# Kernel optimization log

Hardware: AMD Instinct MI355X
Metric: run time of the kernel (lower is better)

The kernel has to match this reference:

```python
import jax, jax.numpy as jnp
import numpy as np

BN_EPS = 1e-5


def setup_inputs() -> dict:
    key = jax.random.key(0)
    ks = jax.random.split(key, 10)
    d = {}
    # EEG-style input: [B, 1, T, electrodes]
    d["x"] = jax.random.normal(ks[0], (512, 1, 1125, 5), dtype=jnp.float32)
    # conv_time: Conv2d(1, 40, (25, 1)) with bias
    d["conv_time_w"] = jax.random.normal(ks[1], (40, 1, 25, 1), dtype=jnp.float32) * 0.05
    d["conv_time_b"] = jax.random.normal(ks[2], (40,), dtype=jnp.float32) * 0.05
    # conv_spat: Conv2d(40, 40, (1, 5), bias=False)
    d["conv_spat_w"] = jax.random.normal(ks[3], (40, 40, 1, 5), dtype=jnp.float32) * 0.05
    # BatchNorm2d(40), eval mode (running stats)
    d["bn_gamma"] = jnp.ones((40,), jnp.float32)
    d["bn_beta"] = jnp.zeros((40,), jnp.float32)
    d["bn_mean"] = jnp.zeros((40,), jnp.float32)
    d["bn_var"] = jnp.ones((40,), jnp.float32)
    # LSTM(input=40, hidden=10): torch layout W_ih [4H, in], W_hh [4H, H]
    d["w_ih"] = jax.random.normal(ks[4], (40, 40), dtype=jnp.float32) * 0.1
    d["w_hh"] = jax.random.normal(ks[5], (40, 10), dtype=jnp.float32) * 0.1
    d["b_ih"] = jax.random.normal(ks[6], (40,), dtype=jnp.float32) * 0.1
    d["b_hh"] = jax.random.normal(ks[7], (40,), dtype=jnp.float32) * 0.1
    # classifier: Linear(10, 2)
    d["fc_w"] = jax.random.normal(ks[8], (2, 10), dtype=jnp.float32) * 0.1
    d["fc_b"] = jnp.zeros((2,), jnp.float32)
    return d


def reference(x, conv_time_w, conv_time_b, conv_spat_w,
              bn_gamma, bn_beta, bn_mean, bn_var,
              w_ih, w_hh, b_ih, b_hh, fc_w, fc_b):
    dn = ("NCHW", "OIHW", "NCHW")
    # conv over time: [B,1,T,5] -> [B,40,T-24,5]
    h = jax.lax.conv_general_dilated(x, conv_time_w, (1, 1), "VALID", dimension_numbers=dn)
    h = h + conv_time_b[None, :, None, None]
    # conv over electrodes: [B,40,T-24,5] -> [B,40,T-24,1]
    h = jax.lax.conv_general_dilated(h, conv_spat_w, (1, 1), "VALID", dimension_numbers=dn)
    # BatchNorm2d (eval, running stats)
    scale = bn_gamma / jnp.sqrt(bn_var + BN_EPS)
    h = h * scale[None, :, None, None] + (bn_beta - bn_mean * scale)[None, :, None, None]
    # AvgPool2d kernel (25,1) stride (5,1): -> [B,40,L,1], L = (T-24-25)//5 + 1
    h = jax.lax.reduce_window(h, 0.0, jax.lax.add, (1, 1, 25, 1), (1, 1, 5, 1), "VALID") / 25.0
    # Dropout2d in eval mode = identity
    # squeeze width + transpose(1,2): [B,40,L] -> [B,L,40]
    h = jnp.transpose(h[..., 0], (0, 2, 1))
    B = h.shape[0]
    H = w_hh.shape[1]  # hidden = 10
    # precompute input-to-gate projection for all timesteps: [L, B, 4H]
    xg = jnp.einsum("blf,gf->lbg", h, w_ih) + b_ih + b_hh

    def step(carry, xt):
        h_prev, c_prev = carry
        gates = xt + h_prev @ w_hh.T          # [B, 4H]
        i, f, g, o = jnp.split(gates, 4, axis=-1)
        i = jax.nn.sigmoid(i)
        f = jax.nn.sigmoid(f)
        g = jnp.tanh(g)
        o = jax.nn.sigmoid(o)
        c = f * c_prev + i * g
        hn = o * jnp.tanh(c)
        return (hn, c), None

    init = (jnp.zeros((B, H), h.dtype), jnp.zeros((B, H), h.dtype))
    (h_last, _), _ = jax.lax.scan(step, init, xg)  # return_seq=False -> last hidden
    return h_last @ fc_w.T + fc_b  # [B, 2]
```

## Files before the change

### kernel.cpp

```cpp
#include <hip/hip_runtime.h>

#define LOG2E 1.44269504088896340736f

typedef float v2f __attribute__((ext_vector_type(2)));

__device__ __forceinline__ float bf2f(unsigned short u) {
    union { unsigned u32; float f; } v; v.u32 = ((unsigned)u) << 16; return v.f;
}
__device__ __forceinline__ unsigned short f2bf(float f) {
    union { float f; unsigned u32; } v; v.f = f;
    unsigned r = (v.u32 + 0x7FFFu + ((v.u32 >> 16) & 1u)) >> 16;
    return (unsigned short)r;
}
__device__ __forceinline__ bool probe_bf16(const void* gma) {
    return *(const unsigned int*)gma == 0x3F803F80u;
}
__device__ __forceinline__ float ldmix(const void* p, int i, bool bf) {
    return bf ? bf2f(((const unsigned short*)p)[i]) : ((const float*)p)[i];
}
__device__ __forceinline__ float dpp_shl(float x, const int n) {
    int r;
    if (n == 1)      r = __builtin_amdgcn_update_dpp(0, __float_as_int(x), 0x101, 0xF, 0xF, true);
    else if (n == 2) r = __builtin_amdgcn_update_dpp(0, __float_as_int(x), 0x102, 0xF, 0xF, true);
    else             r = __builtin_amdgcn_update_dpp(0, __float_as_int(x), 0x103, 0xF, 0xF, true);
    return __int_as_float(r);
}
#if __has_builtin(__builtin_amdgcn_exp2f)
__device__ __forceinline__ float fexp2(float x) { return __builtin_amdgcn_exp2f(x); }
#else
__device__ __forceinline__ float fexp2(float x) {
    float r; asm("v_exp_f32 %0, %1" : "=v"(r) : "v"(x)); return r;
}
#endif

__global__ __launch_bounds__(1024) void prep_kernel(
    const void* __restrict__ ctw,
    const void* __restrict__ ctb,
    const void* __restrict__ csw,
    const void* __restrict__ gma,
    const void* __restrict__ bta,
    const void* __restrict__ mea,
    const void* __restrict__ var,
    const void* __restrict__ wih,
    const void* __restrict__ bih,
    const void* __restrict__ bhh,
    float* __restrict__ Wg,
    float* __restrict__ Bg)
{
    __shared__ float s_wt[1000];
    __shared__ float s_bt[40];
    __shared__ float s_sp[8000];
    __shared__ float s_wih[1600];
    __shared__ float s_scale[40], s_shift[40];
    __shared__ float s_Wc[5000];
    __shared__ float s_P[5200];
    __shared__ float s_Bc[40];
    __shared__ float s_Wp[9920];

    const int t = threadIdx.x;
    const bool bf = probe_bf16(gma);

    for (int i = t; i < 1000; i += 1024) s_wt[i] = ldmix(ctw, i, bf);
    for (int i = t; i < 8000; i += 1024) s_sp[i] = ldmix(csw, i, bf);
    for (int i = t; i < 1600; i += 1024) s_wih[i] = ldmix(wih, i, bf);
    if (t < 40) {
        s_bt[t] = ldmix(ctb, t, bf);
        float sc = ldmix(gma, t, bf) * rsqrtf(ldmix(var, t, bf) + 1e-5f);
        s_scale[t] = sc;
        s_shift[t] = ldmix(bta, t, bf) - ldmix(mea, t, bf) * sc;
    }
    __syncthreads();

    if (t < 200) {
        const int oc = t / 5, kq = (t % 5) * 5;
        float acc[5][5];
        #pragma unroll
        for (int q = 0; q < 5; ++q)
            #pragma unroll
            for (int e = 0; e < 5; ++e) acc[q][e] = 0.f;
        for (int ic = 0; ic < 40; ++ic) {
            float wtv[5], spv[5];
            #pragma unroll
            for (int q = 0; q < 5; ++q) wtv[q] = s_wt[ic * 25 + kq + q];
            #pragma unroll
            for (int e = 0; e < 5; ++e) spv[e] = s_sp[(oc * 40 + ic) * 5 + e];
            #pragma unroll
            for (int q = 0; q < 5; ++q)
                #pragma unroll
                for (int e = 0; e < 5; ++e) acc[q][e] = fmaf(wtv[q], spv[e], acc[q][e]);
        }
        const float sc = s_scale[oc];
        #pragma unroll
        for (int q = 0; q < 5; ++q)
            #pragma unroll
            for (int e = 0; e < 5; ++e)
                s_Wc[(oc * 25 + kq + q) * 5 + e] = acc[q][e] * sc;
    }
    if (t >= 512 && t < 552) {
        const int oc = t - 512;
        float a = 0.f;
        for (int ic = 0; ic < 40; ++ic) {
            float se = 0.f;
            #pragma unroll
            for (int e = 0; e < 5; ++e) se += s_sp[(oc * 40 + ic) * 5 + e];
            a = fmaf(se, s_bt[ic], a);
        }
        s_Bc[oc] = a * s_scale[oc] + s_shift[oc];
    }
    __syncthreads();

    if (t < 200) {
        const int oc = t / 5, e = t % 5;
        float run = 0.f;
        s_P[oc * 130 + e] = 0.f;
        for (int k = 0; k < 25; ++k) {
            run += s_Wc[(oc * 25 + k) * 5 + e];
            s_P[oc * 130 + (k + 1) * 5 + e] = run;
        }
    }
    __syncthreads();

    for (int i = t; i < 9800; i += 1024) {
        const int oc = i / 245, rem = i % 245, j = rem / 5, e = rem % 5;
        const int lo = j - 24 > 0 ? j - 24 : 0;
        const int hi = j < 24 ? j : 24;
        float val = (s_P[oc * 130 + (hi + 1) * 5 + e] - s_P[oc * 130 + lo * 5 + e]) * 0.04f;
        s_Wp[oc * 248 + rem] = val;
    }
    if (t < 120) s_Wp[(t / 3) * 248 + 245 + (t % 3)] = 0.f;
    __syncthreads();

    if (t < 620) {
        const int gp = t / 31, ko = t % 31;
        const int g0 = 2 * gp, kf0 = 8 * ko;
        float acc0[8], acc1[8];
        #pragma unroll
        for (int q = 0; q < 8; ++q) { acc0[q] = 0.f; acc1[q] = 0.f; }
        for (int oc = 0; oc < 40; ++oc) {
            const float4 pa = *reinterpret_cast<const float4*>(&s_Wp[oc * 248 + kf0]);
            const float4 pb = *reinterpret_cast<const float4*>(&s_Wp[oc * 248 + kf0 + 4]);
            const float wa = s_wih[g0 * 40 + oc];
            const float wb = s_wih[(g0 + 1) * 40 + oc];
            acc0[0] = fmaf(wa, pa.x, acc0[0]); acc0[1] = fmaf(wa, pa.y, acc0[1]);
            acc0[2] = fmaf(wa, pa.z, acc0[2]); acc0[3] = fmaf(wa, pa.w, acc0[3]);
            acc0[4] = fmaf(wa, pb.x, acc0[4]); acc0[5] = fmaf(wa, pb.y, acc0[5]);
            acc0[6] = fmaf(wa, pb.z, acc0[6]); acc0[7] = fmaf(wa, pb.w, acc0[7]);
            acc1[0] = fmaf(wb, pa.x, acc1[0]); acc1[1] = fmaf(wb, pa.y, acc1[1]);
            acc1[2] = fmaf(wb, pa.z, acc1[2]); acc1[3] = fmaf(wb, pa.w, acc1[3]);
            acc1[4] = fmaf(wb, pb.x, acc1[4]); acc1[5] = fmaf(wb, pb.y, acc1[5]);
            acc1[6] = fmaf(wb, pb.z, acc1[6]); acc1[7] = fmaf(wb, pb.w, acc1[7]);
        }
        #pragma unroll
        for (int q = 0; q < 8; ++q) {
            Wg[g0 * 248 + kf0 + q]       = acc0[q];
            Wg[(g0 + 1) * 248 + kf0 + q] = acc1[q];
        }
    }
    if (t >= 640 && t < 680) {
        const int g = t - 640;
        float a = ldmix(bih, g, bf) + ldmix(bhh, g, bf);
        for (int oc = 0; oc < 40; ++oc) a = fmaf(s_wih[g * 40 + oc], s_Bc[oc], a);
        Bg[g] = a;
    }
}

__global__ __launch_bounds__(256, 2) void conv_kernel(
    const void* __restrict__ x,
    const float* __restrict__ Wg,
    const float* __restrict__ Bg,
    const void* __restrict__ gma,
    float* __restrict__ xg)
{
    __shared__ float sw[9920];
    __shared__ float u[9184];

    const int b   = blockIdx.x;
    const int tid = threadIdx.x;
    const bool bf = probe_bf16(gma);

    for (int i = tid; i < 9920; i += 256) sw[i] = Wg[i];
    if (bf) {
        const unsigned short* xp = (const unsigned short*)x + b * 5625;
        for (int i = tid; i < 5625; i += 256) u[i] = bf2f(xp[i]);
    } else {
        const float* xp = (const float*)x + b * 5625;
        for (int i = tid; i < 5625; i += 256) u[i] = xp[i];
    }
    for (int i = 5625 + tid; i < 6144; i += 256) u[i] = 0.f;
    __syncthreads();

    const int wave  = __builtin_amdgcn_readfirstlane(tid >> 6);
    const int lane  = tid & 63;
    const int gb    = 20 * (wave & 1);
    const int lbase = 108 * (wave >> 1);
    const int l0 = lbase + lane;
    const int l1 = l0 + 64;
    const int a0 = 25 * l0, a1 = 25 * l1;

    v2f acc[20];
    #pragma unroll
    for (int gi = 0; gi < 20; ++gi) {
        float bgv = Bg[gb + gi];
        acc[gi] = (v2f){bgv, bgv};
    }

    const int wrow = gb * 248;
    for (int k = 0; k < 248; k += 4) {
        v2f xv0 = (v2f){ u[a0 + k],     u[a1 + k]     };
        v2f xv1 = (v2f){ u[a0 + k + 1], u[a1 + k + 1] };
        v2f xv2 = (v2f){ u[a0 + k + 2], u[a1 + k + 2] };
        v2f xv3 = (v2f){ u[a0 + k + 3], u[a1 + k + 3] };
        #pragma unroll
        for (int gi = 0; gi < 20; ++gi) {
            const float4 w = *reinterpret_cast<const float4*>(&sw[wrow + gi * 248 + k]);
            acc[gi] += xv0 * w.x;
            acc[gi] += xv1 * w.y;
            acc[gi] += xv2 * w.z;
            acc[gi] += xv3 * w.w;
        }
    }
    __syncthreads();

    for (int i = 8856 + tid; i < 9184; i += 256) u[i] = 0.f;
    #pragma unroll
    for (int gi = 0; gi < 20; ++gi) {
        const int g = gb + gi;
        const int t = g / 10, q = g - 10 * t;
        const int p = 4 * q + t;
        const float km = (t == 2) ? 2.0f * LOG2E : -LOG2E;
        u[l0 * 41 + p] = km * acc[gi].x;
        if (lane < 44) u[l1 * 41 + p] = km * acc[gi].y;
    }
    __syncthreads();

    float* dst = xg + b * 8960;
    for (int i = tid; i < 8960; i += 256)
        dst[i] = u[(i / 40) * 41 + (i % 40)];
}

__global__ __launch_bounds__(256) void lstm_kernel(
    const float* __restrict__ xg,
    const void* __restrict__ whh_p,
    const void* __restrict__ fcw_p,
    const void* __restrict__ fcb_p,
    const void* __restrict__ gma,
    void* __restrict__ out)
{
    const int tid  = threadIdx.x;
    const int wave = __builtin_amdgcn_readfirstlane(tid >> 6);
    const int lane = tid & 63;
    const int b    = blockIdx.x * 4 + wave;
    const bool bf  = probe_bf16(gma);

    const int m  = lane < 40 ? lane : 39;
    const int j  = m >> 2;
    const int t  = m & 3;
    const int gl = 10 * t + j;

    const float L2   = 2.0f * LOG2E;
    const float kmul = (t == 2) ?  L2 : -LOG2E;
    const float aact = (t == 2) ? -2.0f : (t == 0 ? L2 : 1.0f);
    const float bact = (t == 2) ?  1.0f : 0.0f;

    float whhr[10];
    #pragma unroll
    for (int mm = 0; mm < 10; ++mm) whhr[mm] = kmul * ldmix(whh_p, gl * 10 + mm, bf);

    const float* xp = xg + b * 8960 + m;
    float xb[6];
    #pragma unroll
    for (int p = 0; p < 6; ++p) xb[p] = xp[p * 40];

    float cs = 0.f, h = 0.f;

    for (int l = 0; l < 216; l += 6) {
        #pragma unroll
        for (int s = 0; s < 6; ++s) {
            float xv = xb[s];
            xb[s] = xp[(l + s + 6) * 40];
            float h0 = __int_as_float(__builtin_amdgcn_readlane(__float_as_int(h), 0));
            float h1 = __int_as_float(__builtin_amdgcn_readlane(__float_as_int(h), 4));
            float h2 = __int_as_float(__builtin_amdgcn_readlane(__float_as_int(h), 8));
            float h3 = __int_as_float(__builtin_amdgcn_readlane(__float_as_int(h), 12));
            float h4 = __int_as_float(__builtin_amdgcn_readlane(__float_as_int(h), 16));
            float h5 = __int_as_float(__builtin_amdgcn_readlane(__float_as_int(h), 20));
            float h6 = __int_as_float(__builtin_amdgcn_readlane(__float_as_int(h), 24));
            float h7 = __int_as_float(__builtin_amdgcn_readlane(__float_as_int(h), 28));
            float h8 = __int_as_float(__builtin_amdgcn_readlane(__float_as_int(h), 32));
            float h9 = __int_as_float(__builtin_amdgcn_readlane(__float_as_int(h), 36));
            float a_ = fmaf(whhr[0], h0, xv);
            a_ = fmaf(whhr[1], h1, a_);
            a_ = fmaf(whhr[2], h2, a_);
            float b_ = whhr[3] * h3;
            b_ = fmaf(whhr[4], h4, b_);
            b_ = fmaf(whhr[5], h5, b_);
            float c_ = whhr[6] * h6;
            c_ = fmaf(whhr[7], h7, c_);
            float d_ = whhr[8] * h8;
            d_ = fmaf(whhr[9], h9, d_);
            float accg = (a_ + b_) + (c_ + d_);
            float tt  = fexp2(accg);
            float rr  = __builtin_amdgcn_rcpf(1.0f + tt);
            float act = fmaf(aact, rr, bact);
            float fv = dpp_shl(act, 1);
            float gv = dpp_shl(act, 2);
            float ov = dpp_shl(act, 3);
            cs = fmaf(fv, cs, act * gv);
            float t2 = fexp2(cs);
            float r2 = __builtin_amdgcn_rcpf(1.0f + t2);
            float th = fmaf(-2.0f, r2, 1.0f);
            h = ov * th;
        }
    }

    float w0[10], w1[10];
    #pragma unroll
    for (int mm = 0; mm < 10; ++mm) {
        w0[mm] = ldmix(fcw_p, mm, bf);
        w1[mm] = ldmix(fcw_p, 10 + mm, bf);
    }
    float o0 = ldmix(fcb_p, 0, bf), o1 = ldmix(fcb_p, 1, bf);
    #pragma unroll
    for (int mm = 0; mm < 10; ++mm) {
        float hm = __int_as_float(__builtin_amdgcn_readlane(__float_as_int(h), 4 * mm));
        o0 = fmaf(w0[mm], hm, o0);
        o1 = fmaf(w1[mm], hm, o1);
    }
    if (lane == 0) {
        if (bf) {
            ((unsigned short*)out)[b * 2]     = f2bf(o0);
            ((unsigned short*)out)[b * 2 + 1] = f2bf(o1);
        } else {
            ((float*)out)[b * 2]     = o0;
            ((float*)out)[b * 2 + 1] = o1;
        }
    }
}

__global__ __launch_bounds__(256, 2) void fused_kernel(
    const void* __restrict__ x,
    const float* __restrict__ Wg,
    const float* __restrict__ Bg,
    const void* __restrict__ whh_p,
    const void* __restrict__ fcw_p,
    const void* __restrict__ fcb_p,
    const void* __restrict__ gma,
    void* __restrict__ out)
{
    __shared__ float sw[9920];
    __shared__ float u[8960];

    const int b   = blockIdx.x;
    const int tid = threadIdx.x;
    const bool bf = probe_bf16(gma);

    for (int i = tid; i < 9920; i += 256) sw[i] = Wg[i];
    if (bf) {
        const unsigned short* xp = (const unsigned short*)x + b * 5625;
        for (int i = tid; i < 5625; i += 256) u[i] = bf2f(xp[i]);
    } else {
        const float* xp = (const float*)x + b * 5625;
        for (int i = tid; i < 5625; i += 256) u[i] = xp[i];
    }
    for (int i = 5625 + tid; i < 6144; i += 256) u[i] = 0.f;
    for (int i = 8640 + tid; i < 8960; i += 256) u[i] = 0.f;
    __syncthreads();

    const int wave  = __builtin_amdgcn_readfirstlane(tid >> 6);
    const int lane  = tid & 63;
    const int gb    = 20 * (wave & 1);
    const int lbase = 108 * (wave >> 1);
    const int l0 = lbase + lane;
    const int l1 = l0 + 64;
    const int a0 = 25 * l0, a1 = 25 * l1;

    v2f acc[20];
    #pragma unroll
    for (int gi = 0; gi < 20; ++gi) {
        float bgv = Bg[gb + gi];
        acc[gi] = (v2f){bgv, bgv};
    }

    const int wrow = gb * 248;
    for (int k = 0; k < 248; k += 4) {
        v2f xv0 = (v2f){ u[a0 + k],     u[a1 + k]     };
        v2f xv1 = (v2f){ u[a0 + k + 1], u[a1 + k + 1] };
        v2f xv2 = (v2f){ u[a0 + k + 2], u[a1 + k + 2] };
        v2f xv3 = (v2f){ u[a0 + k + 3], u[a1 + k + 3] };
        #pragma unroll
        for (int gi = 0; gi < 20; ++gi) {
            const float4 w = *reinterpret_cast<const float4*>(&sw[wrow + gi * 248 + k]);
            acc[gi] += xv0 * w.x;
            acc[gi] += xv1 * w.y;
            acc[gi] += xv2 * w.z;
            acc[gi] += xv3 * w.w;
        }
    }
    __syncthreads();

    #pragma unroll
    for (int gi = 0; gi < 20; ++gi) {
        u[l0 * 40 + gb + gi] = acc[gi].x;
        if (lane < 44) u[l1 * 40 + gb + gi] = acc[gi].y;
    }
    __syncthreads();

    if (wave != 0) return;

    const int j   = lane >> 2;
    const int jt  = lane & 3;
    const int jj  = j < 10 ? j : 9;
    const int gl  = 10 * jt + jj;

    const float L2   = 2.0f * LOG2E;
    const float kmul = (jt == 2) ?  L2 : -LOG2E;
    const float aact = (jt == 2) ? -2.0f : (jt == 0 ? L2 : 1.0f);
    const float bact = (jt == 2) ?  1.0f : 0.0f;

    float whhr[10];
    #pragma unroll
    for (int m = 0; m < 10; ++m) whhr[m] = kmul * ldmix(whh_p, gl * 10 + m, bf);

    float xb[6];
    #pragma unroll
    for (int p = 0; p < 6; ++p) xb[p] = kmul * u[p * 40 + gl];

    float cs = 0.f, h = 0.f;

    for (int l = 0; l < 216; l += 6) {
        #pragma unroll
        for (int s = 0; s < 6; ++s) {
            float xv = xb[s];
            xb[s] = kmul * u[(l + s + 6) * 40 + gl];
            float a_ = xv, b_ = 0.f;
            #pragma unroll
            for (int m = 0; m < 10; m += 2) {
                float h0 = __int_as_float(__builtin_amdgcn_readlane(__float_as_int(h), 4 * m));
                float h1 = __int_as_float(__builtin_amdgcn_readlane(__float_as_int(h), 4 * (m + 1)));
                a_ = fmaf(whhr[m], h0, a_);
                b_ = fmaf(whhr[m + 1], h1, b_);
            }
            float accg = a_ + b_;
            float tt  = fexp2(accg);
            float rr  = __builtin_amdgcn_rcpf(1.0f + tt);
            float act = fmaf(aact, rr, bact);
            float fv = dpp_shl(act, 1);
            float gv = dpp_shl(act, 2);
            float ov = dpp_shl(act, 3);
            cs = fmaf(fv, cs, act * gv);
            float t2 = fexp2(cs);
            float r2 = __builtin_amdgcn_rcpf(1.0f + t2);
            float th = fmaf(-2.0f, r2, 1.0f);
            h = ov * th;
        }
    }

    float w0[10], w1[10];
    #pragma unroll
    for (int m = 0; m < 10; ++m) {
        w0[m] = ldmix(fcw_p, m, bf);
        w1[m] = ldmix(fcw_p, 10 + m, bf);
    }
    float o0 = ldmix(fcb_p, 0, bf), o1 = ldmix(fcb_p, 1, bf);
    #pragma unroll
    for (int m = 0; m < 10; ++m) {
        float hm = __int_as_float(__builtin_amdgcn_readlane(__float_as_int(h), 4 * m));
        o0 = fmaf(w0[m], hm, o0);
        o1 = fmaf(w1[m], hm, o1);
    }
    if (lane == 0) {
        if (bf) {
            ((unsigned short*)out)[b * 2]     = f2bf(o0);
            ((unsigned short*)out)[b * 2 + 1] = f2bf(o1);
        } else {
            ((float*)out)[b * 2]     = o0;
            ((float*)out)[b * 2 + 1] = o1;
        }
    }
}

extern "C" void kernel_launch(void* const* d_in, const int* in_sizes, int n_in,
                              void* d_out, int out_size, void* d_ws, size_t ws_size,
                              hipStream_t stream) {
    const void* x    = d_in[0];
    const void* ctw  = d_in[1];
    const void* ctb  = d_in[2];
    const void* csw  = d_in[3];
    const void* gma  = d_in[4];
    const void* bta  = d_in[5];
    const void* mea  = d_in[6];
    const void* var  = d_in[7];
    const void* wih  = d_in[8];
    const void* whh  = d_in[9];
    const void* bih  = d_in[10];
    const void* bhh  = d_in[11];
    const void* fcw  = d_in[12];
    const void* fcb  = d_in[13];

    char* ws = (char*)d_ws;
    float* Wg = (float*)ws;
    float* Bg = (float*)(ws + 40 * 248 * 4);
    float* xg = (float*)(ws + 40960);

    const size_t need = 40960u + 512u * 224u * 40u * 4u;

    prep_kernel<<<1, 1024, 0, stream>>>(ctw, ctb, csw, gma, bta, mea, var,
                                        wih, bih, bhh, Wg, Bg);
    if (ws_size >= need) {
        conv_kernel<<<512, 256, 0, stream>>>(x, Wg, Bg, gma, xg);
        lstm_kernel<<<128, 256, 0, stream>>>(xg, whh, fcw, fcb, gma, d_out);
    } else {
        fused_kernel<<<512, 256, 0, stream>>>(x, Wg, Bg, whh, fcw, fcb, gma, d_out);
    }
}
```

Before: 166.8 us.

## Widen conv register tile to four time positions and deepen LSTM prefetch

The conv kernel drops to 128 threads per block, and each lane now accumulates four pooled time positions instead of two. Each weight float4 read from shared memory is therefore reused across more outputs, which cuts LDS traffic per FMA. The xg buffer is padded to 232 rows per batch, and the LSTM input prefetch ring grows from 6 to 12 steps to hide more global-load latency in the serial recurrence. The costs are higher register pressure, fewer waves per block for hiding latency, and a larger workspace requirement.

```diff
diff --git a/kernel.cpp b/kernel.cpp
--- a/kernel.cpp
+++ b/kernel.cpp
@@ -3,6 +3,7 @@
 #define LOG2E 1.44269504088896340736f
 
 typedef float v2f __attribute__((ext_vector_type(2)));
+typedef float v4f __attribute__((ext_vector_type(4)));
 
 __device__ __forceinline__ float bf2f(unsigned short u) {
     union { unsigned u32; float f; } v; v.u32 = ((unsigned)u) << 16; return v.f;
@@ -164,7 +165,7 @@
     }
 }
 
-__global__ __launch_bounds__(256, 2) void conv_kernel(
+__global__ __launch_bounds__(128) void conv_kernel(
     const void* __restrict__ x,
     const float* __restrict__ Wg,
     const float* __restrict__ Bg,
@@ -172,44 +173,48 @@
     float* __restrict__ xg)
 {
     __shared__ float sw[9920];
-    __shared__ float u[9184];
+    __shared__ float u[8856];
 
     const int b   = blockIdx.x;
     const int tid = threadIdx.x;
     const bool bf = probe_bf16(gma);
 
-    for (int i = tid; i < 9920; i += 256) sw[i] = Wg[i];
+    {
+        const float4* wsrc = reinterpret_cast<const float4*>(Wg);
+        float4* wdst = reinterpret_cast<float4*>(sw);
+        for (int i = tid; i < 2480; i += 128) wdst[i] = wsrc[i];
+    }
     if (bf) {
         const unsigned short* xp = (const unsigned short*)x + b * 5625;
-        for (int i = tid; i < 5625; i += 256) u[i] = bf2f(xp[i]);
+        for (int i = tid; i < 5625; i += 128) u[i] = bf2f(xp[i]);
     } else {
         const float* xp = (const float*)x + b * 5625;
-        for (int i = tid; i < 5625; i += 256) u[i] = xp[i];
-    }
-    for (int i = 5625 + tid; i < 6144; i += 256) u[i] = 0.f;
-    __syncthreads();
-
-    const int wave  = __builtin_amdgcn_readfirstlane(tid >> 6);
-    const int lane  = tid & 63;
-    const int gb    = 20 * (wave & 1);
-    const int lbase = 108 * (wave >> 1);
-    const int l0 = lbase + lane;
-    const int l1 = l0 + 64;
-    const int a0 = 25 * l0, a1 = 25 * l1;
-
-    v2f acc[20];
+        for (int i = tid; i < 5625; i += 128) u[i] = xp[i];
+    }
+    for (int i = 5625 + tid; i < 6144; i += 128) u[i] = 0.f;
+    __syncthreads();
+
+    const int wave = __builtin_amdgcn_readfirstlane(tid >> 6);
+    const int lane = tid & 63;
+    const int gb   = 20 * wave;
+    const int a0 = 25 * lane;
+    const int a1 = 25 * (lane + 54);
+    const int a2 = 25 * (lane + 108);
+    const int a3 = 25 * (lane + 162);
+
+    v4f acc[20];
     #pragma unroll
     for (int gi = 0; gi < 20; ++gi) {
         float bgv = Bg[gb + gi];
-        acc[gi] = (v2f){bgv, bgv};
+        acc[gi] = (v4f){bgv, bgv, bgv, bgv};
     }
 
     const int wrow = gb * 248;
     for (int k = 0; k < 248; k += 4) {
-        v2f xv0 = (v2f){ u[a0 + k],     u[a1 + k]     };
-        v2f xv1 = (v2f){ u[a0 + k + 1], u[a1 + k + 1] };
-        v2f xv2 = (v2f){ u[a0 + k + 2], u[a1 + k + 2] };
-        v2f xv3 = (v2f){ u[a0 + k + 3], u[a1 + k + 3] };
+        v4f xv0 = (v4f){ u[a0 + k],     u[a1 + k],     u[a2 + k],     u[a3 + k]     };
+        v4f xv1 = (v4f){ u[a0 + k + 1], u[a1 + k + 1], u[a2 + k + 1], u[a3 + k + 1] };
+        v4f xv2 = (v4f){ u[a0 + k + 2], u[a1 + k + 2], u[a2 + k + 2], u[a3 + k + 2] };
+        v4f xv3 = (v4f){ u[a0 + k + 3], u[a1 + k + 3], u[a2 + k + 3], u[a3 + k + 3] };
         #pragma unroll
         for (int gi = 0; gi < 20; ++gi) {
             const float4 w = *reinterpret_cast<const float4*>(&sw[wrow + gi * 248 + k]);
@@ -221,21 +226,26 @@
     }
     __syncthreads();
 
-    for (int i = 8856 + tid; i < 9184; i += 256) u[i] = 0.f;
-    #pragma unroll
-    for (int gi = 0; gi < 20; ++gi) {
-        const int g = gb + gi;
-        const int t = g / 10, q = g - 10 * t;
-        const int p = 4 * q + t;
-        const float km = (t == 2) ? 2.0f * LOG2E : -LOG2E;
-        u[l0 * 41 + p] = km * acc[gi].x;
-        if (lane < 44) u[l1 * 41 + p] = km * acc[gi].y;
-    }
-    __syncthreads();
-
-    float* dst = xg + b * 8960;
-    for (int i = tid; i < 8960; i += 256)
-        dst[i] = u[(i / 40) * 41 + (i % 40)];
+    if (lane < 54) {
+        #pragma unroll
+        for (int gi = 0; gi < 20; ++gi) {
+            const int g = gb + gi;
+            const int t = g / 10, q = g - 10 * t;
+            const int p = 4 * q + t;
+            const float km = (t == 2) ? 2.0f * LOG2E : -LOG2E;
+            u[lane * 41 + p]         = km * acc[gi].x;
+            u[(lane + 54) * 41 + p]  = km * acc[gi].y;
+            u[(lane + 108) * 41 + p] = km * acc[gi].z;
+            u[(lane + 162) * 41 + p] = km * acc[gi].w;
+        }
+    }
+    __syncthreads();
+
+    float* dst = xg + b * 9280;
+    for (int i = tid; i < 9280; i += 128) {
+        const int row = i / 40, col = i - 40 * row;
+        dst[i] = (row < 216) ? u[row * 41 + col] : 0.f;
+    }
 }
 
 __global__ __launch_bounds__(256) void lstm_kernel(
@@ -266,18 +276,18 @@
     #pragma unroll
     for (int mm = 0; mm < 10; ++mm) whhr[mm] = kmul * ldmix(whh_p, gl * 10 + mm, bf);
 
-    const float* xp = xg + b * 8960 + m;
-    float xb[6];
-    #pragma unroll
-    for (int p = 0; p < 6; ++p) xb[p] = xp[p * 40];
+    const float* xp = xg + b * 9280 + m;
+    float xb[12];
+    #pragma unroll
+    for (int p = 0; p < 12; ++p) xb[p] = xp[p * 40];
 
     float cs = 0.f, h = 0.f;
 
-    for (int l = 0; l < 216; l += 6) {
-        #pragma unroll
-        for (int s = 0; s < 6; ++s) {
+    for (int l = 0; l < 216; l += 12) {
+        #pragma unroll
+        for (int s = 0; s < 12; ++s) {
             float xv = xb[s];
-            xb[s] = xp[(l + s + 6) * 40];
+            xb[s] = xp[(l + s + 12) * 40];
             float h0 = __int_as_float(__builtin_amdgcn_readlane(__float_as_int(h), 0));
             float h1 = __int_as_float(__builtin_amdgcn_readlane(__float_as_int(h), 4));
             float h2 = __int_as_float(__builtin_amdgcn_readlane(__float_as_int(h), 8));
@@ -502,12 +512,12 @@
     float* Bg = (float*)(ws + 40 * 248 * 4);
     float* xg = (float*)(ws + 40960);
 
-    const size_t need = 40960u + 512u * 224u * 40u * 4u;
+    const size_t need = 40960u + 512u * 232u * 40u * 4u;
 
     prep_kernel<<<1, 1024, 0, stream>>>(ctw, ctb, csw, gma, bta, mea, var,
                                         wih, bih, bhh, Wg, Bg);
     if (ws_size >= need) {
-        conv_kernel<<<512, 256, 0, stream>>>(x, Wg, Bg, gma, xg);
+        conv_kernel<<<512, 128, 0, stream>>>(x, Wg, Bg, gma, xg);
         lstm_kernel<<<128, 256, 0, stream>>>(xg, whh, fcw, fcb, gma, d_out);
     } else {
         fused_kernel<<<512, 256, 0, stream>>>(x, Wg, Bg, whh, fcw, fcb, gma, d_out);
```

Result: slower. 181.2 us (+8.7%).
